# Kernel optimization log

Measured on AMD Instinct MI355X. Metric: run time of the kernel, lower is better.

The kernel has to match this reference:

```python
import jax, jax.numpy as jnp
import numpy as np

TEMPERATURE = 0.07


def setup_inputs() -> dict:
    key = jax.random.key(0)
    k1, k2, k3 = jax.random.split(key, 3)
    B, K, D = 256, 512, 1024
    return {
        "bg_img_feature": jax.random.normal(k1, (B, D), dtype=jnp.float32),
        "fg_pro_feature": jax.random.normal(k2, (B, D), dtype=jnp.float32),
        "bg_pro_feature": jax.random.normal(k3, (B, K, D), dtype=jnp.float32),
    }


def reference(bg_img_feature, fg_pro_feature, bg_pro_feature):
    # Normalize only the background image features (as in the torch module).
    bg_img = bg_img_feature / jnp.linalg.norm(bg_img_feature, axis=-1, keepdims=True)
    # Per-sample logits against K background prototypes: [B, K]
    bg_logits = jnp.einsum("bd,bkd->bk", bg_img, bg_pro_feature)
    # Per-sample logit against its own foreground prototype: [B]
    fg_logits = jnp.sum(bg_img * fg_pro_feature, axis=-1)
    inv_t = 1.0 / TEMPERATURE
    # positive_sims = sum_i mean_k exp(bg_logits[i,k] / T)
    pos = jnp.sum(jnp.mean(jnp.exp(bg_logits * inv_t), axis=-1))
    # negative_sims = pos + sum_i exp(fg_logits[i] / T)
    neg = pos + jnp.sum(jnp.exp(fg_logits * inv_t))
    return -jnp.log(pos / neg)
```

## Files before the change

### kernel.cpp

```cpp
#include <hip/hip_runtime.h>
#include <math.h>

#define B_N 256
#define K_N 512
#define D_N 1024
#define INV_T 14.285714285714286

typedef float vf4 __attribute__((ext_vector_type(4)));


__global__ __launch_bounds__(256) void dot_exp_fused(
    const float* __restrict__ bg_img, const float* __restrict__ fg_pro,
    const float* __restrict__ bg_pro,
    double* __restrict__ block_part, double* __restrict__ fg_part)
{
  const int lane  = threadIdx.x & 63;
  const int wib   = threadIdx.x >> 6;
  const int gwave = blockIdx.x * 4 + wib;
  const int r0    = gwave * 4;
  const int b     = r0 >> 9;

  const vf4* a4 = (const vf4*)(bg_img + (size_t)b * D_N);
  const vf4 a0 = a4[lane];
  const vf4 a1 = a4[lane + 64];
  const vf4 a2 = a4[lane + 128];
  const vf4 a3 = a4[lane + 192];

  const vf4* p4 = (const vf4*)(bg_pro + (size_t)r0 * D_N);
  vf4 x0[4], x1[4], x2[4], x3[4];
  #pragma unroll
  for (int j = 0; j < 4; ++j) {
    const vf4* r = p4 + j * 256;
    x0[j] = __builtin_nontemporal_load(r + lane);
    x1[j] = __builtin_nontemporal_load(r + lane + 64);
    x2[j] = __builtin_nontemporal_load(r + lane + 128);
    x3[j] = __builtin_nontemporal_load(r + lane + 192);
  }

  float ss;
  {
    vf4 m = a0 * a0 + a1 * a1 + a2 * a2 + a3 * a3;
    ss = (m.x + m.y) + (m.z + m.w);
  }

  float s[4];
  #pragma unroll
  for (int j = 0; j < 4; ++j) {
    vf4 m = a0 * x0[j] + a1 * x1[j] + a2 * x2[j] + a3 * x3[j];
    s[j] = (m.x + m.y) + (m.z + m.w);
  }

  #pragma unroll
  for (int off = 32; off > 0; off >>= 1) {
    ss   += __shfl_xor(ss,   off);
    s[0] += __shfl_xor(s[0], off);
    s[1] += __shfl_xor(s[1], off);
    s[2] += __shfl_xor(s[2], off);
    s[3] += __shfl_xor(s[3], off);
  }

  const double inv   = 1.0 / sqrt((double)ss);
  const float  scale = (float)(inv * INV_T);

  const double e = (double)expf(s[0] * scale) + (double)expf(s[1] * scale)
                 + (double)expf(s[2] * scale) + (double)expf(s[3] * scale);

  if ((r0 & (K_N - 1)) == 0) {
    const vf4* f4 = (const vf4*)(fg_pro + (size_t)b * D_N);
    vf4 m = a0 * f4[lane] + a1 * f4[lane + 64]
          + a2 * f4[lane + 128] + a3 * f4[lane + 192];
    float fs = (m.x + m.y) + (m.z + m.w);
    #pragma unroll
    for (int off = 32; off > 0; off >>= 1) fs += __shfl_xor(fs, off);
    if (lane == 0) fg_part[b] = exp((double)fs * inv * INV_T);
  }

  __shared__ double wacc[4];
  if (lane == 0) wacc[wib] = e;
  __syncthreads();
  if (threadIdx.x == 0)
    block_part[blockIdx.x] = (wacc[0] + wacc[1]) + (wacc[2] + wacc[3]);
}

__global__ __launch_bounds__(256) void finalize_kernel(
    const double* __restrict__ block_part, const double* __restrict__ fg_part,
    float* __restrict__ out)
{
  const int t = threadIdx.x;
  double v = 0.0;
  #pragma unroll
  for (int i = 0; i < 32; ++i) v += block_part[t + 256 * i];
  double f = fg_part[t];
  #pragma unroll
  for (int off = 32; off > 0; off >>= 1) {
    v += __shfl_xor(v, off);
    f += __shfl_xor(f, off);
  }
  __shared__ double wv[4], wf[4];
  const int w = t >> 6;
  if ((t & 63) == 0) { wv[w] = v; wf[w] = f; }
  __syncthreads();
  if (t == 0) {
    double pos = ((wv[0] + wv[1]) + (wv[2] + wv[3])) / (double)K_N;
    double fg  = (wf[0] + wf[1]) + (wf[2] + wf[3]);
    out[0] = (float)log1p(fg / pos);
  }
}

extern "C" void kernel_launch(void* const* d_in, const int* in_sizes, int n_in,
                              void* d_out, int out_size, void* d_ws, size_t ws_size,
                              hipStream_t stream) {
  const float* bg_img = (const float*)d_in[0];
  const float* fg_pro = (const float*)d_in[1];
  const float* bg_pro = (const float*)d_in[2];

  char* ws = (char*)d_ws;
  double* block_part = (double*)(ws);
  double* fg_part    = (double*)(ws + 65536);

  dot_exp_fused<<<(B_N * K_N) / 16, 256, 0, stream>>>(
      bg_img, fg_pro, bg_pro, block_part, fg_part);
  finalize_kernel<<<1, 256, 0, stream>>>(block_part, fg_part, (float*)d_out);
}
```

Measured before the change: 647.1 us.

## Fuse finalize via cooperative grid sync and give each wave 32 rows

Each wave now loops over 32 prototype rows instead of 4, so the grid shrinks to 1024 blocks and the per-wave load and norm of the image vector is amortised. The separate finalize launch is folded into the main kernel through a cooperative launch with a grid-wide sync, and block 0 does the final reduction. This removes a kernel launch and most block-level partial writes. In exchange the loop is not unrolled, so fewer loads are in flight per wave to hide HBM latency, and it depends on cooperative launch support, falling back to the two-kernel path otherwise.

```diff
diff --git a/kernel.cpp b/kernel.cpp
--- a/kernel.cpp
+++ b/kernel.cpp
@@ -1,4 +1,5 @@
 #include <hip/hip_runtime.h>
+#include <hip/hip_cooperative_groups.h>
 #include <math.h>
 
 #define B_N 256
@@ -8,16 +9,23 @@
 
 typedef float vf4 __attribute__((ext_vector_type(4)));
 
+namespace cg = cooperative_groups;
 
-__global__ __launch_bounds__(256) void dot_exp_fused(
+
+template <bool COOP>
+__global__ __launch_bounds__(256, 4) void infonce_fused(
     const float* __restrict__ bg_img, const float* __restrict__ fg_pro,
     const float* __restrict__ bg_pro,
-    double* __restrict__ block_part, double* __restrict__ fg_part)
+    double* __restrict__ block_part, double* __restrict__ fg_part,
+    float* __restrict__ out)
 {
+  __shared__ double wacc[4];
+  __shared__ double wv[4], wf[4];
+
   const int lane  = threadIdx.x & 63;
   const int wib   = threadIdx.x >> 6;
   const int gwave = blockIdx.x * 4 + wib;
-  const int r0    = gwave * 4;
+  const int r0    = gwave * 32;
   const int b     = r0 >> 9;
 
   const vf4* a4 = (const vf4*)(bg_img + (size_t)b * D_N);
@@ -26,60 +34,81 @@
   const vf4 a2 = a4[lane + 128];
   const vf4 a3 = a4[lane + 192];
 
-  const vf4* p4 = (const vf4*)(bg_pro + (size_t)r0 * D_N);
-  vf4 x0[4], x1[4], x2[4], x3[4];
+  float ss;
+  { vf4 m = a0*a0 + a1*a1 + a2*a2 + a3*a3; ss = (m.x+m.y)+(m.z+m.w); }
   #pragma unroll
-  for (int j = 0; j < 4; ++j) {
-    const vf4* r = p4 + j * 256;
-    x0[j] = __builtin_nontemporal_load(r + lane);
-    x1[j] = __builtin_nontemporal_load(r + lane + 64);
-    x2[j] = __builtin_nontemporal_load(r + lane + 128);
-    x3[j] = __builtin_nontemporal_load(r + lane + 192);
-  }
-
-  float ss;
-  {
-    vf4 m = a0 * a0 + a1 * a1 + a2 * a2 + a3 * a3;
-    ss = (m.x + m.y) + (m.z + m.w);
-  }
-
-  float s[4];
-  #pragma unroll
-  for (int j = 0; j < 4; ++j) {
-    vf4 m = a0 * x0[j] + a1 * x1[j] + a2 * x2[j] + a3 * x3[j];
-    s[j] = (m.x + m.y) + (m.z + m.w);
-  }
-
-  #pragma unroll
-  for (int off = 32; off > 0; off >>= 1) {
-    ss   += __shfl_xor(ss,   off);
-    s[0] += __shfl_xor(s[0], off);
-    s[1] += __shfl_xor(s[1], off);
-    s[2] += __shfl_xor(s[2], off);
-    s[3] += __shfl_xor(s[3], off);
-  }
-
+  for (int off = 32; off > 0; off >>= 1) ss += __shfl_xor(ss, off);
   const double inv   = 1.0 / sqrt((double)ss);
   const float  scale = (float)(inv * INV_T);
 
-  const double e = (double)expf(s[0] * scale) + (double)expf(s[1] * scale)
-                 + (double)expf(s[2] * scale) + (double)expf(s[3] * scale);
-
   if ((r0 & (K_N - 1)) == 0) {
     const vf4* f4 = (const vf4*)(fg_pro + (size_t)b * D_N);
-    vf4 m = a0 * f4[lane] + a1 * f4[lane + 64]
-          + a2 * f4[lane + 128] + a3 * f4[lane + 192];
-    float fs = (m.x + m.y) + (m.z + m.w);
+    vf4 m = a0*f4[lane] + a1*f4[lane+64] + a2*f4[lane+128] + a3*f4[lane+192];
+    float fs = (m.x+m.y)+(m.z+m.w);
     #pragma unroll
     for (int off = 32; off > 0; off >>= 1) fs += __shfl_xor(fs, off);
     if (lane == 0) fg_part[b] = exp((double)fs * inv * INV_T);
   }
 
-  __shared__ double wacc[4];
-  if (lane == 0) wacc[wib] = e;
+  double acc = 0.0;
+  const vf4* p4 = (const vf4*)(bg_pro + (size_t)r0 * D_N);
+  #pragma unroll 1
+  for (int q = 0; q < 8; ++q) {
+    const vf4* r = p4 + q * 1024;
+    vf4 x0[4], x1[4], x2[4], x3[4];
+    #pragma unroll
+    for (int j = 0; j < 4; ++j) {
+      const vf4* rj = r + j * 256;
+      x0[j] = __builtin_nontemporal_load(rj + lane);
+      x1[j] = __builtin_nontemporal_load(rj + lane + 64);
+      x2[j] = __builtin_nontemporal_load(rj + lane + 128);
+      x3[j] = __builtin_nontemporal_load(rj + lane + 192);
+    }
+    float s[4];
+    #pragma unroll
+    for (int j = 0; j < 4; ++j) {
+      vf4 m = a0*x0[j] + a1*x1[j] + a2*x2[j] + a3*x3[j];
+      s[j] = (m.x+m.y)+(m.z+m.w);
+    }
+    #pragma unroll
+    for (int off = 32; off > 0; off >>= 1) {
+      s[0] += __shfl_xor(s[0], off);
+      s[1] += __shfl_xor(s[1], off);
+      s[2] += __shfl_xor(s[2], off);
+      s[3] += __shfl_xor(s[3], off);
+    }
+    acc += (double)expf(s[0]*scale) + (double)expf(s[1]*scale)
+         + (double)expf(s[2]*scale) + (double)expf(s[3]*scale);
+  }
+
+  if (lane == 0) wacc[wib] = acc;
   __syncthreads();
   if (threadIdx.x == 0)
-    block_part[blockIdx.x] = (wacc[0] + wacc[1]) + (wacc[2] + wacc[3]);
+    block_part[blockIdx.x] = (wacc[0]+wacc[1])+(wacc[2]+wacc[3]);
+
+  if constexpr (COOP) {
+    __threadfence();
+    cg::this_grid().sync();
+    if (blockIdx.x == 0) {
+      const int t = threadIdx.x;
+      double v = block_part[t] + block_part[t + 256]
+               + block_part[t + 512] + block_part[t + 768];
+      double f = fg_part[t];
+      #pragma unroll
+      for (int off = 32; off > 0; off >>= 1) {
+        v += __shfl_xor(v, off);
+        f += __shfl_xor(f, off);
+      }
+      const int w = t >> 6;
+      if ((t & 63) == 0) { wv[w] = v; wf[w] = f; }
+      __syncthreads();
+      if (t == 0) {
+        double pos = ((wv[0]+wv[1])+(wv[2]+wv[3])) / (double)K_N;
+        double fg  = (wf[0]+wf[1])+(wf[2]+wf[3]);
+        out[0] = (float)log1p(fg / pos);
+      }
+    }
+  }
 }
 
 __global__ __launch_bounds__(256) void finalize_kernel(
@@ -87,9 +116,8 @@
     float* __restrict__ out)
 {
   const int t = threadIdx.x;
-  double v = 0.0;
-  #pragma unroll
-  for (int i = 0; i < 32; ++i) v += block_part[t + 256 * i];
+  double v = block_part[t] + block_part[t + 256]
+           + block_part[t + 512] + block_part[t + 768];
   double f = fg_part[t];
   #pragma unroll
   for (int off = 32; off > 0; off >>= 1) {
@@ -101,8 +129,8 @@
   if ((t & 63) == 0) { wv[w] = v; wf[w] = f; }
   __syncthreads();
   if (t == 0) {
-    double pos = ((wv[0] + wv[1]) + (wv[2] + wv[3])) / (double)K_N;
-    double fg  = (wf[0] + wf[1]) + (wf[2] + wf[3]);
+    double pos = ((wv[0]+wv[1])+(wv[2]+wv[3])) / (double)K_N;
+    double fg  = (wf[0]+wf[1])+(wf[2]+wf[3]);
     out[0] = (float)log1p(fg / pos);
   }
 }
@@ -116,9 +144,33 @@
 
   char* ws = (char*)d_ws;
   double* block_part = (double*)(ws);
-  double* fg_part    = (double*)(ws + 65536);
+  double* fg_part    = (double*)(ws + 8192);
+  float*  outf       = (float*)d_out;
 
-  dot_exp_fused<<<(B_N * K_N) / 16, 256, 0, stream>>>(
-      bg_img, fg_pro, bg_pro, block_part, fg_part);
-  finalize_kernel<<<1, 256, 0, stream>>>(block_part, fg_part, (float*)d_out);
+  static int coop_ok = -1;
+  if (coop_ok < 0) {
+    int v = 0;
+    coop_ok = (hipDeviceGetAttribute(&v, hipDeviceAttributeCooperativeLaunch, 0)
+               == hipSuccess) ? v : 0;
+  }
+
+  bool launched = false;
+  if (coop_ok) {
+    void* args[] = { (void*)&bg_img, (void*)&fg_pro, (void*)&bg_pro,
+                     (void*)&block_part, (void*)&fg_part, (void*)&outf };
+    hipError_t err = hipLaunchCooperativeKernel(
+        reinterpret_cast<const void*>(&infonce_fused<true>),
+        dim3(1024), dim3(256), args, 0, stream);
+    if (err == hipSuccess) {
+      launched = true;
+    } else {
+      (void)hipGetLastError();
+      coop_ok = 0;
+    }
+  }
+  if (!launched) {
+    infonce_fused<false><<<1024, 256, 0, stream>>>(
+        bg_img, fg_pro, bg_pro, block_part, fg_part, outf);
+    finalize_kernel<<<1, 256, 0, stream>>>(block_part, fg_part, outf);
+  }
 }
```

Result: slower. 817.1 us (+26.3%).
